# Kernel tuning notes

Measured on AMD Instinct MI355X. Metric: run time of the kernel, lower is better.

The kernel has to match this reference:

```python
import jax, jax.numpy as jnp
import numpy as np

N, T, P = 4096, 4096, 12  # series, timesteps, seasonality period


def setup_inputs() -> dict:
    key = jax.random.key(0)
    ks = jax.random.split(key, 8)
    return {
        "alpha": jax.random.uniform(ks[0], (N,), dtype=jnp.float32),
        "beta": jax.random.uniform(ks[1], (N,), dtype=jnp.float32),
        "gamma": jax.random.uniform(ks[2], (N,), dtype=jnp.float32),
        "init_level": jax.random.normal(ks[3], (N,), dtype=jnp.float32),
        "init_trend": jax.random.normal(ks[4], (N,), dtype=jnp.float32) * 0.01,
        "init_seasonal": jax.random.normal(ks[5], (N, P), dtype=jnp.float32),
        "obs_noise": jax.random.normal(ks[6], (N, T), dtype=jnp.float32),
        "err": jax.random.normal(ks[7], (N, T), dtype=jnp.float32),
    }


def reference(alpha, beta, gamma, init_level, init_trend, init_seasonal, obs_noise, err):
    """ETS 'AAA' (additive error/trend/seasonal) recurrence, vectorized over N series.

    Per timestep t (matching the torch loop with model_type='AAA'):
      current = level + trend + seasonal[t % P]
      y[t]    = current + obs_noise[t] * 0.1
      level'  = alpha*(current + err[t]) + (1-alpha)*(level + trend)
      trend'  = beta*(level' - level) + (1-beta)*trend
      seasonal[t % P] = gamma*err[t] + (1-gamma)*seasonal[t % P]
    """
    Tlen = obs_noise.shape[1]
    Pn = init_seasonal.shape[1]

    def step(carry, xs):
        level, trend, seasonal = carry  # (N,), (N,), (N, P)
        t, on, e = xs                   # scalar, (N,), (N,)
        idx = t % Pn
        s_t = seasonal[:, idx]
        current = level + trend + s_t
        y = current + on * 0.1
        new_level = alpha * (current + e) + (1.0 - alpha) * (level + trend)
        new_trend = beta * (new_level - level) + (1.0 - beta) * trend
        new_seasonal = seasonal.at[:, idx].set(gamma * e + (1.0 - gamma) * s_t)
        return (new_level, new_trend, new_seasonal), y

    xs = (jnp.arange(Tlen), obs_noise.T, err.T)  # scan over time
    _, ys = jax.lax.scan(step, (init_level, init_trend, init_seasonal), xs)
    return ys.T  # (N, T)
```

## Files before the change

kernel.cpp:

```cpp
#include <hip/hip_runtime.h>

#define DEV static __device__ __forceinline__

#define SKEW4(j) ((j) + (((j) >> 7) << 2))

DEV float elem(const float4& v, int j) {
  switch (j & 3) {
    case 0: return v.x;
    case 1: return v.y;
    case 2: return v.z;
    default: return v.w;
  }
}
DEV void setelem(float4& v, int j, float x) {
  switch (j & 3) {
    case 0: v.x = x; break;
    case 1: v.y = x; break;
    case 2: v.z = x; break;
    default: v.w = x; break;
  }
}

__global__ __launch_bounds__(128) void ets_hb(
    const float* __restrict__ alpha_, const float* __restrict__ beta_,
    const float* __restrict__ gamma_, const float* __restrict__ lvl0,
    const float* __restrict__ tr0, const float* __restrict__ seas0,
    const float* __restrict__ obs, const float* __restrict__ err,
    float* __restrict__ out, int T)
{
  __shared__ __align__(16) float er_s[2436];
  __shared__ float tot[20];

  const int n = blockIdx.x;
  const int tid = threadIdx.x;
  const int lane = tid & 63;
  const int wv = tid >> 6;

  const float4* ER4 = reinterpret_cast<const float4*>(err + (size_t)n * T);
  const float4* OB4 = reinterpret_cast<const float4*>(obs + (size_t)n * T);
  const int nf4 = T >> 2;

  const int nper = T / 12;
  const int base = nper >> 7, rem = nper & 127;
  const int m  = base + (tid < rem ? 1 : 0);
  const int p0 = tid * base + min(tid, rem);
  const int t0 = p0 * 12;

  const int pSplit = 64 * base + min(64, rem);
  const int R0 = pSplit * 12;
  const int R0f4 = R0 >> 2;

  for (int i = tid; i < R0f4; i += 128) {
    *reinterpret_cast<float4*>(&er_s[SKEW4(i << 2)]) = ER4[i];
  }
  __syncthreads();

  float4 E[9];
  if (wv == 0) {
    int t = t0;
#pragma unroll
    for (int u = 0; u < 3; ++u, t += 12) {
      if (u < m) {
        E[u * 3 + 0] = *reinterpret_cast<const float4*>(&er_s[SKEW4(t)]);
        E[u * 3 + 1] = *reinterpret_cast<const float4*>(&er_s[SKEW4(t + 4)]);
        E[u * 3 + 2] = *reinterpret_cast<const float4*>(&er_s[SKEW4(t + 8)]);
      }
    }
  }
  __syncthreads();

  for (int i = R0f4 + tid; i < nf4; i += 128) {
    *reinterpret_cast<float4*>(&er_s[SKEW4((i << 2) - R0)]) = ER4[i];
  }
  __syncthreads();

  if (wv == 1) {
    int t = t0 - R0;
#pragma unroll
    for (int u = 0; u < 3; ++u, t += 12) {
      if (u < m) {
        E[u * 3 + 0] = *reinterpret_cast<const float4*>(&er_s[SKEW4(t)]);
        E[u * 3 + 1] = *reinterpret_cast<const float4*>(&er_s[SKEW4(t + 4)]);
        E[u * 3 + 2] = *reinterpret_cast<const float4*>(&er_s[SKEW4(t + 8)]);
      }
    }
  }

  const float a = alpha_[n], b = beta_[n], g = gamma_[n];
  const float ab = a * b, ig = 1.0f - g;

  float l = 0.f, tr = 0.f, s[12];
#pragma unroll
  for (int j = 0; j < 12; ++j) s[j] = 0.f;
#pragma unroll
  for (int u = 0; u < 3; ++u) {
    if (u < m) {
#pragma unroll
      for (int j = 0; j < 12; ++j) {
        float e = elem(E[u * 3 + (j >> 2)], j);
        float se = s[j] + e;
        float lt = l + tr;
        l  = fmaf(a, se, lt);
        tr = fmaf(ab, se, tr);
        s[j] = fmaf(g, e, ig * s[j]);
      }
    }
  }

  float S0 = 0.f, S1 = 0.f, dk = 1.f;
  for (int k = 0; k < m; ++k) { S0 += dk; S1 += (float)k * dk; dk *= ig; }
  float GL = 12.0f * (float)m;
  float Gd = dk;
  float Gf = ab * S0;
  float GA = fmaf(a, S0, ab * ((GL - 1.0f) * S0 - 12.0f * S1));
  float Pl = l, Pt = tr, Ps[12];
#pragma unroll
  for (int j = 0; j < 12; ++j) Ps[j] = s[j];

#pragma unroll
  for (int dlt = 1; dlt < 64; dlt <<= 1) {
    float oL  = __shfl_up(GL, dlt, 64);
    float od  = __shfl_up(Gd, dlt, 64);
    float of  = __shfl_up(Gf, dlt, 64);
    float oA  = __shfl_up(GA, dlt, 64);
    float oPl = __shfl_up(Pl, dlt, 64);
    float oPt = __shfl_up(Pt, dlt, 64);
    float oPs[12];
#pragma unroll
    for (int j = 0; j < 12; ++j) oPs[j] = __shfl_up(Ps[j], dlt, 64);
    if (lane >= dlt) {
      float S = 0.f, W = 0.f;
#pragma unroll
      for (int j = 0; j < 12; ++j) {
        S += oPs[j];
        W = fmaf((float)j, oPs[j], W);
      }
      float dot = GA * S - Gf * W;
      float nPl = oPl + GL * oPt + dot + Pl;
      float nPt = fmaf(Gf, S, oPt) + Pt;
#pragma unroll
      for (int j = 0; j < 12; ++j) Ps[j] = fmaf(Gd, oPs[j], Ps[j]);
      GA = oA + GL * of + GA * od;
      Pl = nPl; Pt = nPt;
      Gf = of + Gf * od;
      Gd = od * Gd;
      GL = oL + GL;
    }
  }

  if (wv == 0 && lane == 63) {
    tot[0] = GL; tot[1] = Gd; tot[2] = Gf; tot[3] = GA; tot[4] = Pl; tot[5] = Pt;
#pragma unroll
    for (int j = 0; j < 12; ++j) tot[6 + j] = Ps[j];
  }
  __syncthreads();

  float xl = lvl0[n], xt = tr0[n], xs[12];
#pragma unroll
  for (int j = 0; j < 12; ++j) xs[j] = seas0[(size_t)n * 12 + j];
  if (wv == 1) {
    float ss = 0.f, sw = 0.f;
#pragma unroll
    for (int j = 0; j < 12; ++j) {
      ss += xs[j];
      sw = fmaf((float)j, xs[j], sw);
    }
    float cdot = tot[3] * ss - tot[2] * sw;
    float nxl = xl + tot[0] * xt + cdot + tot[4];
    float nxt = fmaf(tot[2], ss, xt) + tot[5];
#pragma unroll
    for (int j = 0; j < 12; ++j) xs[j] = fmaf(tot[1], xs[j], tot[6 + j]);
    xl = nxl; xt = nxt;
  }

  float ss = 0.f, sw = 0.f;
#pragma unroll
  for (int j = 0; j < 12; ++j) {
    ss += xs[j];
    sw = fmaf((float)j, xs[j], sw);
  }
  float cdot = GA * ss - Gf * sw;
  float yl = xl + GL * xt + cdot + Pl;
  float yt = fmaf(Gf, ss, xt) + Pt;
  float ys[12];
#pragma unroll
  for (int j = 0; j < 12; ++j) ys[j] = fmaf(Gd, xs[j], Ps[j]);

  l  = __shfl_up(yl, 1, 64);
  tr = __shfl_up(yt, 1, 64);
#pragma unroll
  for (int j = 0; j < 12; ++j) s[j] = __shfl_up(ys[j], 1, 64);
  if (lane == 0) {
    l = xl; tr = xt;
#pragma unroll
    for (int j = 0; j < 12; ++j) s[j] = xs[j];
  }

  auto pass2 = [&](int trel) {
#pragma unroll
    for (int u = 0; u < 3; ++u) {
      if (u < m) {
        float4 y0, y1, y2;
#pragma unroll
        for (int j = 0; j < 12; ++j) {
          float e = elem(E[u * 3 + (j >> 2)], j);
          float lt = l + tr;
          float cur = lt + s[j];
          float4& yd = (j < 4 ? y0 : (j < 8 ? y1 : y2));
          setelem(yd, j, cur);
          float se = s[j] + e;
          l  = fmaf(a, se, lt);
          tr = fmaf(ab, se, tr);
          s[j] = fmaf(g, e, ig * s[j]);
        }
        int t = trel + u * 12;
        *reinterpret_cast<float4*>(&er_s[SKEW4(t)])     = y0;
        *reinterpret_cast<float4*>(&er_s[SKEW4(t + 4)]) = y1;
        *reinterpret_cast<float4*>(&er_s[SKEW4(t + 8)]) = y2;
      }
    }
  };

  if (wv == 1) {
    pass2(t0 - R0);
    if (tid == 127) {
      int tt = nper * 12;
      int tail = T - tt;
#pragma unroll
      for (int j = 0; j < 11; ++j) {
        if (j < tail) {
          int ad = SKEW4(tt - R0 + j);
          float e = er_s[ad];
          float lt = l + tr;
          float cur = lt + s[j];
          er_s[ad] = cur;
          float se = s[j] + e;
          l  = fmaf(a, se, lt);
          tr = fmaf(ab, se, tr);
          s[j] = fmaf(g, e, ig * s[j]);
        }
      }
    }
  }
  __syncthreads();

  float4* Y4 = reinterpret_cast<float4*>(out + (size_t)n * T);
  for (int i = R0f4 + tid; i < nf4; i += 128) {
    float4 o = OB4[i];
    float4 c = *reinterpret_cast<const float4*>(&er_s[SKEW4((i << 2) - R0)]);
    Y4[i] = make_float4(fmaf(o.x, 0.1f, c.x), fmaf(o.y, 0.1f, c.y),
                        fmaf(o.z, 0.1f, c.z), fmaf(o.w, 0.1f, c.w));
  }
  __syncthreads();

  if (wv == 0) pass2(t0);
  __syncthreads();

  for (int i = tid; i < R0f4; i += 128) {
    float4 o = OB4[i];
    float4 c = *reinterpret_cast<const float4*>(&er_s[SKEW4(i << 2)]);
    Y4[i] = make_float4(fmaf(o.x, 0.1f, c.x), fmaf(o.y, 0.1f, c.y),
                        fmaf(o.z, 0.1f, c.z), fmaf(o.w, 0.1f, c.w));
  }
}

__global__ void ets_gen(
    const float* __restrict__ alpha_, const float* __restrict__ beta_,
    const float* __restrict__ gamma_, const float* __restrict__ lvl0,
    const float* __restrict__ tr0, const float* __restrict__ seas0,
    const float* __restrict__ obs, const float* __restrict__ err,
    float* __restrict__ out, int N, int T, int P)
{
  extern __shared__ float smem[];
  int n = blockIdx.x * blockDim.x + threadIdx.x;
  if (n >= N) return;
  float* s = smem + (size_t)threadIdx.x * P;
  for (int j = 0; j < P; ++j) s[j] = seas0[(size_t)n * P + j];

  float a = alpha_[n], b = beta_[n], g = gamma_[n];
  float ia = 1.0f - a, ib = 1.0f - b, ig = 1.0f - g;
  float level = lvl0[n], trend = tr0[n];

  const float* on = obs + (size_t)n * T;
  const float* er = err + (size_t)n * T;
  float*       yo = out + (size_t)n * T;

  int idx = 0;
  for (int t = 0; t < T; ++t) {
    float onj = on[t], ej = er[t];
    float sj  = s[idx];
    float cur = level + trend + sj;
    yo[t] = fmaf(onj, 0.1f, cur);
    float lt  = level + trend;
    float nl  = fmaf(a, cur + ej, ia * lt);
    float nt  = fmaf(b, nl - level, ib * trend);
    s[idx]    = fmaf(g, ej, ig * sj);
    level = nl; trend = nt;
    if (++idx == P) idx = 0;
  }
}

extern "C" void kernel_launch(void* const* d_in, const int* in_sizes, int n_in,
                              void* d_out, int out_size, void* d_ws, size_t ws_size,
                              hipStream_t stream) {
  (void)n_in; (void)out_size; (void)d_ws; (void)ws_size;
  const float* alpha = (const float*)d_in[0];
  const float* beta  = (const float*)d_in[1];
  const float* gamma = (const float*)d_in[2];
  const float* lvl0  = (const float*)d_in[3];
  const float* tr0   = (const float*)d_in[4];
  const float* seas0 = (const float*)d_in[5];
  const float* obs   = (const float*)d_in[6];
  const float* err   = (const float*)d_in[7];
  float* y = (float*)d_out;

  int N = in_sizes[0];
  int P = in_sizes[5] / N;
  int T = in_sizes[6] / N;

  if (P == 12 && (T % 4) == 0 && T >= 12 && T <= 4096) {
    ets_hb<<<dim3(N), dim3(128), 0, stream>>>(
        alpha, beta, gamma, lvl0, tr0, seas0, obs, err, y, T);
  } else {
    int bs = 64;
    size_t sh = (size_t)bs * (size_t)P * sizeof(float);
    ets_gen<<<dim3((N + bs - 1) / bs), dim3(bs), sh, stream>>>(
        alpha, beta, gamma, lvl0, tr0, seas0, obs, err, y, N, T, P);
  }
}
```

Measured before the change: 43.72 us.

## Process two series per block and prefetch the second series' errors into registers

Each block now handles two series sequentially with half as many blocks launched. The err row of the second series is loaded into registers at kernel start so its global latency overlaps the first series' scan. This adds 32 VGPRs per thread and reduces grid size, which may lower occupancy and latency hiding.

New measurement: 72.12 us. 1.65x slower.

```diff
diff --git a/kernel.cpp b/kernel.cpp
--- a/kernel.cpp
+++ b/kernel.cpp
@@ -21,246 +21,285 @@
   }
 }
 
-__global__ __launch_bounds__(128) void ets_hb(
+__global__ __launch_bounds__(128) void ets_pipe(
     const float* __restrict__ alpha_, const float* __restrict__ beta_,
     const float* __restrict__ gamma_, const float* __restrict__ lvl0,
     const float* __restrict__ tr0, const float* __restrict__ seas0,
     const float* __restrict__ obs, const float* __restrict__ err,
-    float* __restrict__ out, int T)
+    float* __restrict__ out, int T, int NB, int N)
 {
   __shared__ __align__(16) float er_s[2436];
   __shared__ float tot[20];
 
-  const int n = blockIdx.x;
   const int tid = threadIdx.x;
   const int lane = tid & 63;
   const int wv = tid >> 6;
 
-  const float4* ER4 = reinterpret_cast<const float4*>(err + (size_t)n * T);
-  const float4* OB4 = reinterpret_cast<const float4*>(obs + (size_t)n * T);
   const int nf4 = T >> 2;
-
   const int nper = T / 12;
   const int base = nper >> 7, rem = nper & 127;
   const int m  = base + (tid < rem ? 1 : 0);
   const int p0 = tid * base + min(tid, rem);
   const int t0 = p0 * 12;
-
   const int pSplit = 64 * base + min(64, rem);
   const int R0 = pSplit * 12;
   const int R0f4 = R0 >> 2;
 
-  for (int i = tid; i < R0f4; i += 128) {
-    *reinterpret_cast<float4*>(&er_s[SKEW4(i << 2)]) = ER4[i];
-  }
-  __syncthreads();
-
-  float4 E[9];
-  if (wv == 0) {
-    int t = t0;
-#pragma unroll
-    for (int u = 0; u < 3; ++u, t += 12) {
+  const int n1 = blockIdx.x + NB;
+  float4 X[8];
+  if (n1 < N) {
+    const float4* ER1 = reinterpret_cast<const float4*>(err + (size_t)n1 * T);
+#pragma unroll
+    for (int k = 0; k < 8; ++k) {
+      int i = tid + (k << 7);
+      if (i < nf4) X[k] = ER1[i];
+    }
+  }
+
+  for (int it = 0; it < 2; ++it) {
+    const int n = blockIdx.x + it * NB;
+    if (n >= N) break;
+
+    const float4* ER4 = reinterpret_cast<const float4*>(err + (size_t)n * T);
+    const float4* OB4 = reinterpret_cast<const float4*>(obs + (size_t)n * T);
+
+    if (it == 0) {
+#pragma unroll
+      for (int k = 0; k < 8; ++k) {
+        int i = tid + (k << 7);
+        if (i < R0f4)
+          *reinterpret_cast<float4*>(&er_s[SKEW4(i << 2)]) = ER4[i];
+      }
+    } else {
+#pragma unroll
+      for (int k = 0; k < 8; ++k) {
+        int i = tid + (k << 7);
+        if (i < R0f4)
+          *reinterpret_cast<float4*>(&er_s[SKEW4(i << 2)]) = X[k];
+      }
+    }
+    __syncthreads();
+
+    float4 E[9];
+    if (wv == 0) {
+      int t = t0;
+#pragma unroll
+      for (int u = 0; u < 3; ++u, t += 12) {
+        if (u < m) {
+          E[u * 3 + 0] = *reinterpret_cast<const float4*>(&er_s[SKEW4(t)]);
+          E[u * 3 + 1] = *reinterpret_cast<const float4*>(&er_s[SKEW4(t + 4)]);
+          E[u * 3 + 2] = *reinterpret_cast<const float4*>(&er_s[SKEW4(t + 8)]);
+        }
+      }
+    }
+    __syncthreads();
+
+    if (it == 0) {
+#pragma unroll
+      for (int k = 0; k < 8; ++k) {
+        int i = tid + (k << 7);
+        if (i >= R0f4 && i < nf4)
+          *reinterpret_cast<float4*>(&er_s[SKEW4((i << 2) - R0)]) = ER4[i];
+      }
+    } else {
+#pragma unroll
+      for (int k = 0; k < 8; ++k) {
+        int i = tid + (k << 7);
+        if (i >= R0f4 && i < nf4)
+          *reinterpret_cast<float4*>(&er_s[SKEW4((i << 2) - R0)]) = X[k];
+      }
+    }
+    __syncthreads();
+
+    if (wv == 1) {
+      int t = t0 - R0;
+#pragma unroll
+      for (int u = 0; u < 3; ++u, t += 12) {
+        if (u < m) {
+          E[u * 3 + 0] = *reinterpret_cast<const float4*>(&er_s[SKEW4(t)]);
+          E[u * 3 + 1] = *reinterpret_cast<const float4*>(&er_s[SKEW4(t + 4)]);
+          E[u * 3 + 2] = *reinterpret_cast<const float4*>(&er_s[SKEW4(t + 8)]);
+        }
+      }
+    }
+
+    const float a = alpha_[n], b = beta_[n], g = gamma_[n];
+    const float ab = a * b, ig = 1.0f - g;
+
+    float l = 0.f, tr = 0.f, s[12];
+#pragma unroll
+    for (int j = 0; j < 12; ++j) s[j] = 0.f;
+#pragma unroll
+    for (int u = 0; u < 3; ++u) {
       if (u < m) {
-        E[u * 3 + 0] = *reinterpret_cast<const float4*>(&er_s[SKEW4(t)]);
-        E[u * 3 + 1] = *reinterpret_cast<const float4*>(&er_s[SKEW4(t + 4)]);
-        E[u * 3 + 2] = *reinterpret_cast<const float4*>(&er_s[SKEW4(t + 8)]);
-      }
-    }
-  }
-  __syncthreads();
-
-  for (int i = R0f4 + tid; i < nf4; i += 128) {
-    *reinterpret_cast<float4*>(&er_s[SKEW4((i << 2) - R0)]) = ER4[i];
-  }
-  __syncthreads();
-
-  if (wv == 1) {
-    int t = t0 - R0;
-#pragma unroll
-    for (int u = 0; u < 3; ++u, t += 12) {
-      if (u < m) {
-        E[u * 3 + 0] = *reinterpret_cast<const float4*>(&er_s[SKEW4(t)]);
-        E[u * 3 + 1] = *reinterpret_cast<const float4*>(&er_s[SKEW4(t + 4)]);
-        E[u * 3 + 2] = *reinterpret_cast<const float4*>(&er_s[SKEW4(t + 8)]);
-      }
-    }
-  }
-
-  const float a = alpha_[n], b = beta_[n], g = gamma_[n];
-  const float ab = a * b, ig = 1.0f - g;
-
-  float l = 0.f, tr = 0.f, s[12];
-#pragma unroll
-  for (int j = 0; j < 12; ++j) s[j] = 0.f;
-#pragma unroll
-  for (int u = 0; u < 3; ++u) {
-    if (u < m) {
+#pragma unroll
+        for (int j = 0; j < 12; ++j) {
+          float e = elem(E[u * 3 + (j >> 2)], j);
+          float se = s[j] + e;
+          float lt = l + tr;
+          l  = fmaf(a, se, lt);
+          tr = fmaf(ab, se, tr);
+          s[j] = fmaf(g, e, ig * s[j]);
+        }
+      }
+    }
+
+    float S0 = 0.f, S1 = 0.f, dk = 1.f;
+    for (int k = 0; k < m; ++k) { S0 += dk; S1 += (float)k * dk; dk *= ig; }
+    float GL = 12.0f * (float)m;
+    float Gd = dk;
+    float Gf = ab * S0;
+    float GA = fmaf(a, S0, ab * ((GL - 1.0f) * S0 - 12.0f * S1));
+    float Pl = l, Pt = tr, Ps[12];
+#pragma unroll
+    for (int j = 0; j < 12; ++j) Ps[j] = s[j];
+
+#pragma unroll
+    for (int dlt = 1; dlt < 64; dlt <<= 1) {
+      float oL  = __shfl_up(GL, dlt, 64);
+      float od  = __shfl_up(Gd, dlt, 64);
+      float of  = __shfl_up(Gf, dlt, 64);
+      float oA  = __shfl_up(GA, dlt, 64);
+      float oPl = __shfl_up(Pl, dlt, 64);
+      float oPt = __shfl_up(Pt, dlt, 64);
+      float oPs[12];
+#pragma unroll
+      for (int j = 0; j < 12; ++j) oPs[j] = __shfl_up(Ps[j], dlt, 64);
+      if (lane >= dlt) {
+        float S = 0.f, W = 0.f;
+#pragma unroll
+        for (int j = 0; j < 12; ++j) {
+          S += oPs[j];
+          W = fmaf((float)j, oPs[j], W);
+        }
+        float dot = GA * S - Gf * W;
+        float nPl = oPl + GL * oPt + dot + Pl;
+        float nPt = fmaf(Gf, S, oPt) + Pt;
+#pragma unroll
+        for (int j = 0; j < 12; ++j) Ps[j] = fmaf(Gd, oPs[j], Ps[j]);
+        GA = oA + GL * of + GA * od;
+        Pl = nPl; Pt = nPt;
+        Gf = of + Gf * od;
+        Gd = od * Gd;
+        GL = oL + GL;
+      }
+    }
+
+    if (wv == 0 && lane == 63) {
+      tot[0] = GL; tot[1] = Gd; tot[2] = Gf; tot[3] = GA; tot[4] = Pl; tot[5] = Pt;
+#pragma unroll
+      for (int j = 0; j < 12; ++j) tot[6 + j] = Ps[j];
+    }
+    __syncthreads();
+
+    float xl = lvl0[n], xt = tr0[n], xs[12];
+#pragma unroll
+    for (int j = 0; j < 12; ++j) xs[j] = seas0[(size_t)n * 12 + j];
+    if (wv == 1) {
+      float ss = 0.f, sw = 0.f;
 #pragma unroll
       for (int j = 0; j < 12; ++j) {
-        float e = elem(E[u * 3 + (j >> 2)], j);
-        float se = s[j] + e;
-        float lt = l + tr;
-        l  = fmaf(a, se, lt);
-        tr = fmaf(ab, se, tr);
-        s[j] = fmaf(g, e, ig * s[j]);
-      }
-    }
-  }
-
-  float S0 = 0.f, S1 = 0.f, dk = 1.f;
-  for (int k = 0; k < m; ++k) { S0 += dk; S1 += (float)k * dk; dk *= ig; }
-  float GL = 12.0f * (float)m;
-  float Gd = dk;
-  float Gf = ab * S0;
-  float GA = fmaf(a, S0, ab * ((GL - 1.0f) * S0 - 12.0f * S1));
-  float Pl = l, Pt = tr, Ps[12];
-#pragma unroll
-  for (int j = 0; j < 12; ++j) Ps[j] = s[j];
-
-#pragma unroll
-  for (int dlt = 1; dlt < 64; dlt <<= 1) {
-    float oL  = __shfl_up(GL, dlt, 64);
-    float od  = __shfl_up(Gd, dlt, 64);
-    float of  = __shfl_up(Gf, dlt, 64);
-    float oA  = __shfl_up(GA, dlt, 64);
-    float oPl = __shfl_up(Pl, dlt, 64);
-    float oPt = __shfl_up(Pt, dlt, 64);
-    float oPs[12];
-#pragma unroll
-    for (int j = 0; j < 12; ++j) oPs[j] = __shfl_up(Ps[j], dlt, 64);
-    if (lane >= dlt) {
-      float S = 0.f, W = 0.f;
-#pragma unroll
-      for (int j = 0; j < 12; ++j) {
-        S += oPs[j];
-        W = fmaf((float)j, oPs[j], W);
-      }
-      float dot = GA * S - Gf * W;
-      float nPl = oPl + GL * oPt + dot + Pl;
-      float nPt = fmaf(Gf, S, oPt) + Pt;
-#pragma unroll
-      for (int j = 0; j < 12; ++j) Ps[j] = fmaf(Gd, oPs[j], Ps[j]);
-      GA = oA + GL * of + GA * od;
-      Pl = nPl; Pt = nPt;
-      Gf = of + Gf * od;
-      Gd = od * Gd;
-      GL = oL + GL;
-    }
-  }
-
-  if (wv == 0 && lane == 63) {
-    tot[0] = GL; tot[1] = Gd; tot[2] = Gf; tot[3] = GA; tot[4] = Pl; tot[5] = Pt;
-#pragma unroll
-    for (int j = 0; j < 12; ++j) tot[6 + j] = Ps[j];
-  }
-  __syncthreads();
-
-  float xl = lvl0[n], xt = tr0[n], xs[12];
-#pragma unroll
-  for (int j = 0; j < 12; ++j) xs[j] = seas0[(size_t)n * 12 + j];
-  if (wv == 1) {
+        ss += xs[j];
+        sw = fmaf((float)j, xs[j], sw);
+      }
+      float cdot = tot[3] * ss - tot[2] * sw;
+      float nxl = xl + tot[0] * xt + cdot + tot[4];
+      float nxt = fmaf(tot[2], ss, xt) + tot[5];
+#pragma unroll
+      for (int j = 0; j < 12; ++j) xs[j] = fmaf(tot[1], xs[j], tot[6 + j]);
+      xl = nxl; xt = nxt;
+    }
+
     float ss = 0.f, sw = 0.f;
 #pragma unroll
     for (int j = 0; j < 12; ++j) {
       ss += xs[j];
       sw = fmaf((float)j, xs[j], sw);
     }
-    float cdot = tot[3] * ss - tot[2] * sw;
-    float nxl = xl + tot[0] * xt + cdot + tot[4];
-    float nxt = fmaf(tot[2], ss, xt) + tot[5];
-#pragma unroll
-    for (int j = 0; j < 12; ++j) xs[j] = fmaf(tot[1], xs[j], tot[6 + j]);
-    xl = nxl; xt = nxt;
-  }
-
-  float ss = 0.f, sw = 0.f;
-#pragma unroll
-  for (int j = 0; j < 12; ++j) {
-    ss += xs[j];
-    sw = fmaf((float)j, xs[j], sw);
-  }
-  float cdot = GA * ss - Gf * sw;
-  float yl = xl + GL * xt + cdot + Pl;
-  float yt = fmaf(Gf, ss, xt) + Pt;
-  float ys[12];
-#pragma unroll
-  for (int j = 0; j < 12; ++j) ys[j] = fmaf(Gd, xs[j], Ps[j]);
-
-  l  = __shfl_up(yl, 1, 64);
-  tr = __shfl_up(yt, 1, 64);
-#pragma unroll
-  for (int j = 0; j < 12; ++j) s[j] = __shfl_up(ys[j], 1, 64);
-  if (lane == 0) {
-    l = xl; tr = xt;
-#pragma unroll
-    for (int j = 0; j < 12; ++j) s[j] = xs[j];
-  }
-
-  auto pass2 = [&](int trel) {
-#pragma unroll
-    for (int u = 0; u < 3; ++u) {
-      if (u < m) {
-        float4 y0, y1, y2;
-#pragma unroll
-        for (int j = 0; j < 12; ++j) {
-          float e = elem(E[u * 3 + (j >> 2)], j);
-          float lt = l + tr;
-          float cur = lt + s[j];
-          float4& yd = (j < 4 ? y0 : (j < 8 ? y1 : y2));
-          setelem(yd, j, cur);
-          float se = s[j] + e;
-          l  = fmaf(a, se, lt);
-          tr = fmaf(ab, se, tr);
-          s[j] = fmaf(g, e, ig * s[j]);
-        }
-        int t = trel + u * 12;
-        *reinterpret_cast<float4*>(&er_s[SKEW4(t)])     = y0;
-        *reinterpret_cast<float4*>(&er_s[SKEW4(t + 4)]) = y1;
-        *reinterpret_cast<float4*>(&er_s[SKEW4(t + 8)]) = y2;
-      }
-    }
-  };
-
-  if (wv == 1) {
-    pass2(t0 - R0);
-    if (tid == 127) {
-      int tt = nper * 12;
-      int tail = T - tt;
-#pragma unroll
-      for (int j = 0; j < 11; ++j) {
-        if (j < tail) {
-          int ad = SKEW4(tt - R0 + j);
-          float e = er_s[ad];
-          float lt = l + tr;
-          float cur = lt + s[j];
-          er_s[ad] = cur;
-          float se = s[j] + e;
-          l  = fmaf(a, se, lt);
-          tr = fmaf(ab, se, tr);
-          s[j] = fmaf(g, e, ig * s[j]);
-        }
-      }
-    }
-  }
-  __syncthreads();
-
-  float4* Y4 = reinterpret_cast<float4*>(out + (size_t)n * T);
-  for (int i = R0f4 + tid; i < nf4; i += 128) {
-    float4 o = OB4[i];
-    float4 c = *reinterpret_cast<const float4*>(&er_s[SKEW4((i << 2) - R0)]);
-    Y4[i] = make_float4(fmaf(o.x, 0.1f, c.x), fmaf(o.y, 0.1f, c.y),
-                        fmaf(o.z, 0.1f, c.z), fmaf(o.w, 0.1f, c.w));
-  }
-  __syncthreads();
-
-  if (wv == 0) pass2(t0);
-  __syncthreads();
-
-  for (int i = tid; i < R0f4; i += 128) {
-    float4 o = OB4[i];
-    float4 c = *reinterpret_cast<const float4*>(&er_s[SKEW4(i << 2)]);
-    Y4[i] = make_float4(fmaf(o.x, 0.1f, c.x), fmaf(o.y, 0.1f, c.y),
-                        fmaf(o.z, 0.1f, c.z), fmaf(o.w, 0.1f, c.w));
+    float cdot = GA * ss - Gf * sw;
+    float yl = xl + GL * xt + cdot + Pl;
+    float yt = fmaf(Gf, ss, xt) + Pt;
+    float ys[12];
+#pragma unroll
+    for (int j = 0; j < 12; ++j) ys[j] = fmaf(Gd, xs[j], Ps[j]);
+
+    l  = __shfl_up(yl, 1, 64);
+    tr = __shfl_up(yt, 1, 64);
+#pragma unroll
+    for (int j = 0; j < 12; ++j) s[j] = __shfl_up(ys[j], 1, 64);
+    if (lane == 0) {
+      l = xl; tr = xt;
+#pragma unroll
+      for (int j = 0; j < 12; ++j) s[j] = xs[j];
+    }
+
+    auto pass2 = [&](int trel) {
+#pragma unroll
+      for (int u = 0; u < 3; ++u) {
+        if (u < m) {
+          float4 y0, y1, y2;
+#pragma unroll
+          for (int j = 0; j < 12; ++j) {
+            float e = elem(E[u * 3 + (j >> 2)], j);
+            float lt = l + tr;
+            float cur = lt + s[j];
+            float4& yd = (j < 4 ? y0 : (j < 8 ? y1 : y2));
+            setelem(yd, j, cur);
+            float se = s[j] + e;
+            l  = fmaf(a, se, lt);
+            tr = fmaf(ab, se, tr);
+            s[j] = fmaf(g, e, ig * s[j]);
+          }
+          int t = trel + u * 12;
+          *reinterpret_cast<float4*>(&er_s[SKEW4(t)])     = y0;
+          *reinterpret_cast<float4*>(&er_s[SKEW4(t + 4)]) = y1;
+          *reinterpret_cast<float4*>(&er_s[SKEW4(t + 8)]) = y2;
+        }
+      }
+    };
+
+    if (wv == 1) {
+      pass2(t0 - R0);
+      if (tid == 127) {
+        int tt = nper * 12;
+        int tail = T - tt;
+#pragma unroll
+        for (int j = 0; j < 11; ++j) {
+          if (j < tail) {
+            int ad = SKEW4(tt - R0 + j);
+            float e = er_s[ad];
+            float lt = l + tr;
+            float cur = lt + s[j];
+            er_s[ad] = cur;
+            float se = s[j] + e;
+            l  = fmaf(a, se, lt);
+            tr = fmaf(ab, se, tr);
+            s[j] = fmaf(g, e, ig * s[j]);
+          }
+        }
+      }
+    }
+    __syncthreads();
+
+    float4* Y4 = reinterpret_cast<float4*>(out + (size_t)n * T);
+    for (int i = R0f4 + tid; i < nf4; i += 128) {
+      float4 o = OB4[i];
+      float4 c = *reinterpret_cast<const float4*>(&er_s[SKEW4((i << 2) - R0)]);
+      Y4[i] = make_float4(fmaf(o.x, 0.1f, c.x), fmaf(o.y, 0.1f, c.y),
+                          fmaf(o.z, 0.1f, c.z), fmaf(o.w, 0.1f, c.w));
+    }
+    __syncthreads();
+
+    if (wv == 0) pass2(t0);
+    __syncthreads();
+
+    for (int i = tid; i < R0f4; i += 128) {
+      float4 o = OB4[i];
+      float4 c = *reinterpret_cast<const float4*>(&er_s[SKEW4(i << 2)]);
+      Y4[i] = make_float4(fmaf(o.x, 0.1f, c.x), fmaf(o.y, 0.1f, c.y),
+                          fmaf(o.z, 0.1f, c.z), fmaf(o.w, 0.1f, c.w));
+    }
+    __syncthreads();
   }
 }
 
@@ -319,8 +358,9 @@
   int T = in_sizes[6] / N;
 
   if (P == 12 && (T % 4) == 0 && T >= 12 && T <= 4096) {
-    ets_hb<<<dim3(N), dim3(128), 0, stream>>>(
-        alpha, beta, gamma, lvl0, tr0, seas0, obs, err, y, T);
+    int NB = (N + 1) / 2;
+    ets_pipe<<<dim3(NB), dim3(128), 0, stream>>>(
+        alpha, beta, gamma, lvl0, tr0, seas0, obs, err, y, T, NB, N);
   } else {
     int bs = 64;
     size_t sh = (size_t)bs * (size_t)P * sizeof(float);
```
